# Kernel optimization log

Measured on AMD Instinct MI355X. Metric: run time of the kernel, lower is better.

## Reference

```python
import jax, jax.numpy as jnp
import numpy as np
from jax import lax

B, CIN, COUT, K, H, W = 16, 512, 512, 3, 64, 64
STYLE_DIM, BASIS, DIRS = 512, 8, 8


def setup_inputs() -> dict:
    key = jax.random.key(0)
    ks = jax.random.split(key, 8)
    return {
        "x": jax.random.normal(ks[0], (B, CIN, H, W), jnp.float32),
        "style": jax.random.normal(ks[1], (B, STYLE_DIM), jnp.float32),
        "weight": jax.random.normal(ks[2], (1, COUT, CIN, K, K), jnp.float32),
        "mod_w": jax.random.normal(ks[3], (CIN, STYLE_DIM), jnp.float32) * 0.02,
        "mod_b": jnp.ones((CIN,), jnp.float32),
        "basis_vectors": jax.random.normal(ks[4], (BASIS, 1, COUT, CIN, K, K), jnp.float32),
        "shifts_coords": jax.random.normal(ks[5], (DIRS, BASIS), jnp.float32),
        "batch_shifts": jax.random.uniform(ks[6], (B,), jnp.float32),
        "batch_directions": jax.random.randint(ks[7], (B,), 0, DIRS),
    }


def reference(x, style, weight, mod_w, mod_b, basis_vectors, shifts_coords,
              batch_shifts, batch_directions):
    batch, in_ch, h, w = x.shape
    out_ch, k = weight.shape[1], weight.shape[3]
    scale = 1.0 / np.sqrt(in_ch * k * k)  # StyleGAN2 equalized-lr scale

    # --- deformation: per-sample weight delta from basis subspace ---
    coefs = shifts_coords[batch_directions]                     # [B, basis]
    bv = basis_vectors.reshape(basis_vectors.shape[0], -1)      # [basis, O*I*k*k]
    delta = coefs @ bv                                          # [B, P]
    nrm = jnp.linalg.norm(delta, axis=1, keepdims=True)
    delta = delta / jnp.maximum(nrm, 1e-12) * batch_shifts[:, None]
    delta = delta.reshape(batch, out_ch, in_ch, k, k)
    wgt = weight + delta                                        # [B, O, I, k, k]

    # --- style modulation + demodulation ---
    s = style @ mod_w.T + mod_b                                 # [B, I]
    wgt = scale * wgt * s[:, None, :, None, None]
    demod = lax.rsqrt(jnp.sum(wgt * wgt, axis=(2, 3, 4)) + 1e-8)  # [B, O]
    wgt = wgt * demod[:, :, None, None, None]

    # --- grouped conv, groups = batch ---
    wgt = wgt.reshape(batch * out_ch, in_ch, k, k)
    xg = x.reshape(1, batch * in_ch, h, w)
    pad = k // 2
    out = lax.conv_general_dilated(
        xg, wgt, window_strides=(1, 1), padding=[(pad, pad), (pad, pad)],
        feature_group_count=batch,
        dimension_numbers=("NCHW", "OIHW", "NCHW"))
    return out.reshape(batch, out_ch, h, w)
```

## Files before the change

kernel.cpp:

```cpp
#include <hip/hip_runtime.h>


typedef __attribute__((ext_vector_type(8))) short bf16x8;
typedef __attribute__((ext_vector_type(4))) float f32x4;

__device__ __forceinline__ unsigned short f2bf(float f) {
  unsigned u = __float_as_uint(f);
  return (unsigned short)((u + 0x7FFFu + ((u >> 16) & 1u)) >> 16);
}

__device__ __forceinline__ void gl_lds16(const void* g, void* l) {
  __builtin_amdgcn_global_load_lds(
      (const __attribute__((address_space(1))) void*)g,
      (__attribute__((address_space(3))) void*)l, 16, 0, 0);
}

template <int N> __device__ __forceinline__ void vm_wait() {
  if constexpr (N == 8) asm volatile("s_waitcnt vmcnt(8)" ::: "memory");
  else if constexpr (N == 0) asm volatile("s_waitcnt vmcnt(0)" ::: "memory");
}

__global__ __launch_bounds__(256) void k_pad(const float* __restrict__ x,
                                             unsigned short* __restrict__ xp) {
  const int bx = blockIdx.x;
  const int b   = bx >> 9;
  const int rem = bx & 511;
  const int y   = rem >> 3;
  const int cb  = rem & 7;
  const int t = threadIdx.x;
  __shared__ float tile[64][65];
  const float* src = x + ((size_t)(b * 512 + cb * 64) * 4096) + y * 64;
#pragma unroll
  for (int r = 0; r < 4; ++r) {
    int idx = r * 256 + t;
    int ch = idx >> 4;
    int xq = (idx & 15) << 2;
    float4 v = *(const float4*)(src + (size_t)ch * 4096 + xq);
    tile[ch][xq + 0] = v.x; tile[ch][xq + 1] = v.y;
    tile[ch][xq + 2] = v.z; tile[ch][xq + 3] = v.w;
  }
  const uint4 z4 = {0u, 0u, 0u, 0u};
  if (t < 16) {
    const int side = t >> 3;
    const int lo = (t & 7) * 8;
    unsigned short* p =
        xp + (((size_t)(b * 66 + y + 1) * 66 + side * 65) * 512 + cb * 64 + lo);
    *(uint4*)p = z4;
  }
  if (y == 0 || y == 63) {
    const int row = (y == 0) ? 0 : 65;
    for (int idx = t; idx < 528; idx += 256) {
      const int c = idx >> 3;
      const int lo = (idx & 7) * 8;
      unsigned short* p =
          xp + (((size_t)(b * 66 + row) * 66 + c) * 512 + cb * 64 + lo);
      *(uint4*)p = z4;
    }
  }
  __syncthreads();
  const int col = t >> 2;
  const int q = t & 3;
  union { unsigned short u16[16]; uint4 v[2]; } pk;
#pragma unroll
  for (int j = 0; j < 16; ++j) pk.u16[j] = f2bf(tile[q * 16 + j][col]);
  unsigned short* dst =
      xp + (((size_t)(b * 66 + y + 1) * 66 + col + 1) * 512 + cb * 64 + q * 16);
  *(uint4*)dst = pk.v[0];
  *(uint4*)(dst + 8) = pk.v[1];
}

__global__ __launch_bounds__(256) void k_mod(const float* __restrict__ style,
                                             const float* __restrict__ mod_w,
                                             const float* __restrict__ mod_b,
                                             float* __restrict__ smod) {
  const int b = blockIdx.x;
  __shared__ float st[512];
  for (int d = threadIdx.x; d < 512; d += 256) st[d] = style[b * 512 + d];
  __syncthreads();
  for (int i = threadIdx.x; i < 512; i += 256) {
    const float* wr = mod_w + (size_t)i * 512;
    float acc = 0.f;
#pragma unroll 4
    for (int d = 0; d < 512; d += 4) {
      float4 wv = *(const float4*)(wr + d);
      acc += wv.x * st[d] + wv.y * st[d + 1] + wv.z * st[d + 2] + wv.w * st[d + 3];
    }
    smod[b * 512 + i] = acc + mod_b[i];
  }
}

__global__ __launch_bounds__(256, 3) void k_gram(const float* __restrict__ bv,
                                                 float* __restrict__ G) {
  const int P4 = 589824;
  float a[36];
#pragma unroll
  for (int c = 0; c < 36; ++c) a[c] = 0.f;
  const float4* bv4 = (const float4*)bv;
  for (int p = blockIdx.x * 256 + threadIdx.x; p < P4; p += gridDim.x * 256) {
    float4 v[8];
#pragma unroll
    for (int k = 0; k < 8; ++k) v[k] = bv4[(size_t)k * P4 + p];
    int c = 0;
#pragma unroll
    for (int i = 0; i < 8; ++i)
#pragma unroll
      for (int j = i; j < 8; ++j) {
        a[c] += v[i].x * v[j].x + v[i].y * v[j].y + v[i].z * v[j].z +
                v[i].w * v[j].w;
        ++c;
      }
  }
#pragma unroll
  for (int c = 0; c < 36; ++c)
#pragma unroll
    for (int off = 32; off > 0; off >>= 1) a[c] += __shfl_down(a[c], off);
  __shared__ float red[4][36];
  const int wv = threadIdx.x >> 6;
  if ((threadIdx.x & 63) == 0)
#pragma unroll
    for (int c = 0; c < 36; ++c) red[wv][c] = a[c];
  __syncthreads();
  if (threadIdx.x < 36)
    atomicAdd(&G[threadIdx.x], red[0][threadIdx.x] + red[1][threadIdx.x] +
                                   red[2][threadIdx.x] + red[3][threadIdx.x]);
}

__global__ void k_amp(const float* __restrict__ shifts_coords,
                      const float* __restrict__ batch_shifts,
                      const int* __restrict__ dirs, const float* __restrict__ G,
                      float* __restrict__ camp) {
  const int b = threadIdx.x;
  if (b < 16) {
    const int dir = dirs[b];
    float c[8];
    for (int k = 0; k < 8; ++k) c[k] = shifts_coords[dir * 8 + k];
    float n2 = 0.f;
    int idx = 0;
    for (int i = 0; i < 8; ++i)
      for (int j = i; j < 8; ++j) {
        float g = G[idx++];
        n2 += (i == j) ? c[i] * c[i] * g : 2.f * c[i] * c[j] * g;
      }
    float nrm = sqrtf(fmaxf(n2, 0.f));
    float amp = batch_shifts[b] / fmaxf(nrm, 1e-12f);
    for (int k = 0; k < 8; ++k) camp[b * 8 + k] = c[k] * amp;
  }
}

__global__ __launch_bounds__(512) void k_weights(const float* __restrict__ weight,
                                                 const float* __restrict__ bv,
                                                 const float* __restrict__ smod,
                                                 const float* __restrict__ camp,
                                                 unsigned short* __restrict__ wgt,
                                                 float* __restrict__ demod) {
  const int o = blockIdx.x;
  const int i = threadIdx.x;
  __shared__ float cl[128];
  __shared__ float red[8][16];
  if (threadIdx.x < 128) cl[threadIdx.x] = camp[threadIdx.x];
  __syncthreads();
  const float scl = 0.014731391274719738f;
  float sm[16];
#pragma unroll
  for (int b = 0; b < 16; ++b) sm[b] = smod[b * 512 + i] * scl;
  float ssq[16];
#pragma unroll
  for (int b = 0; b < 16; ++b) ssq[b] = 0.f;
  const size_t base = ((size_t)o * 512 + i) * 9;
#pragma unroll
  for (int g = 0; g < 3; ++g) {
    float w[3], v[8][3];
#pragma unroll
    for (int q = 0; q < 3; ++q) w[q] = weight[base + g * 3 + q];
#pragma unroll
    for (int k = 0; k < 8; ++k)
#pragma unroll
      for (int q = 0; q < 3; ++q)
        v[k][q] = bv[(size_t)k * 2359296 + base + g * 3 + q];
#pragma unroll
    for (int b = 0; b < 16; ++b) {
#pragma unroll
      for (int q = 0; q < 3; ++q) {
        float d = w[q];
#pragma unroll
        for (int k = 0; k < 8; ++k) d = fmaf(cl[b * 8 + k], v[k][q], d);
        float wv = d * sm[b];
        ssq[b] = fmaf(wv, wv, ssq[b]);
        wgt[(((size_t)(b * 9 + g * 3 + q) * 512 + o) << 9) + i] = f2bf(wv);
      }
    }
  }
#pragma unroll
  for (int b = 0; b < 16; ++b)
#pragma unroll
    for (int off = 32; off > 0; off >>= 1) ssq[b] += __shfl_down(ssq[b], off);
  const int wv_ = threadIdx.x >> 6;
  if ((threadIdx.x & 63) == 0)
#pragma unroll
    for (int b = 0; b < 16; ++b) red[wv_][b] = ssq[b];
  __syncthreads();
  if (threadIdx.x < 16) {
    float s = 0.f;
#pragma unroll
    for (int wq = 0; wq < 8; ++wq) s += red[wq][threadIdx.x];
    demod[threadIdx.x * 512 + o] = rsqrtf(s + 1e-8f);
  }
}

__global__ __launch_bounds__(512, 2) void k_conv(
    const unsigned short* __restrict__ xp, const unsigned short* __restrict__ wgt,
    const float* __restrict__ demod, float* __restrict__ out) {
  extern __shared__ unsigned char smem[];
  const int tid = threadIdx.x;
  const int l = tid & 63;
  const int w = tid >> 6;
  const int wo = w >> 2;
  const int wn = w & 3;

  const int bid = blockIdx.x;
  const int bz = (bid & 7) * 64 + (bid >> 3);
  const int b = bz >> 5;
  const int tt = bz & 31;
  const int o0 = (tt >> 4) << 8;
  const int tn = tt & 15;
  const int n0 = tn << 8;
  const int y0 = tn << 2;

  int swzS[4];
  size_t aByte[4], pBase[4];
#pragma unroll
  for (int r = 0; r < 4; ++r) {
    const int idx = r * 512 + tid;
    const int row = idx >> 3;
    const int swz = ((idx & 7) << 4) ^ ((row & 7) << 4);
    swzS[r] = swz;
    aByte[r] = ((size_t)(o0 + row) << 10) + swz;
    pBase[r] = (size_t)(b * 66 + y0 + (row >> 6)) * 66 + (row & 63);
  }

  const char* wgtc = (const char*)wgt;
  const char* xpc = (const char*)xp;

  auto stage_part = [&](unsigned char* buf, int kt, int part) {
    const int kk = kt >> 3;
    const int is = kt & 7;
    const int ky = kk / 3;
    const int kx = kk - ky * 3;
    const size_t aPlane = ((size_t)(b * 9 + kk) << 19) + ((size_t)is << 7);
    unsigned char* lA = buf;
    unsigned char* lB = buf + 32768;
    if (part == 0) {
#pragma unroll
      for (int r = 0; r < 2; ++r)
        gl_lds16(wgtc + aPlane + aByte[r], lA + (r * 512 + tid) * 16);
#pragma unroll
      for (int r = 0; r < 2; ++r)
        gl_lds16(xpc + (((pBase[r] + ky * 66 + kx) << 10) + ((size_t)is << 7) +
                        swzS[r]),
                 lB + (r * 512 + tid) * 16);
    } else if (part == 1) {
#pragma unroll
      for (int r = 2; r < 4; ++r)
        gl_lds16(xpc + (((pBase[r] + ky * 66 + kx) << 10) + ((size_t)is << 7) +
                        swzS[r]),
                 lB + (r * 512 + tid) * 16);
    } else {
#pragma unroll
      for (int r = 2; r < 4; ++r)
        gl_lds16(wgtc + aPlane + aByte[r], lA + (r * 512 + tid) * 16);
    }
  };

  f32x4 acc[8][4];
  const f32x4 zz = {0.f, 0.f, 0.f, 0.f};
#pragma unroll
  for (int mi = 0; mi < 8; ++mi)
#pragma unroll
    for (int ni = 0; ni < 4; ++ni) acc[mi][ni] = zz;
  bf16x8 af[8], bf0[4], bf1[4];

  auto rdA = [&](const unsigned char* lA, int MH) {
#pragma unroll
    for (int mi = 0; mi < 4; ++mi)
#pragma unroll
      for (int ks = 0; ks < 2; ++ks) {
        const int row = MH * 128 + wo * 64 + mi * 16 + (l & 15);
        af[mi * 2 + ks] = *(const bf16x8*)(
            lA + row * 128 + ((ks * 64 + ((l >> 4) << 4)) ^ ((row & 7) << 4)));
      }
  };
  auto rdB = [&](const unsigned char* lB, int NH, bf16x8 (&bfx)[4]) {
#pragma unroll
    for (int ni = 0; ni < 2; ++ni)
#pragma unroll
      for (int ks = 0; ks < 2; ++ks) {
        const int row = NH * 128 + wn * 32 + ni * 16 + (l & 15);
        bfx[ni * 2 + ks] = *(const bf16x8*)(
            lB + row * 128 + ((ks * 64 + ((l >> 4) << 4)) ^ ((row & 7) << 4)));
      }
  };
  auto mma = [&](int MH, int NH, bf16x8 (&bfx)[4]) {
    __builtin_amdgcn_s_setprio(1);
#pragma unroll
    for (int mi = 0; mi < 4; ++mi)
#pragma unroll
      for (int ni = 0; ni < 2; ++ni)
#pragma unroll
        for (int ks = 0; ks < 2; ++ks)
          acc[MH * 4 + mi][NH * 2 + ni] =
              __builtin_amdgcn_mfma_f32_16x16x32_bf16(
                  af[mi * 2 + ks], bfx[ni * 2 + ks],
                  acc[MH * 4 + mi][NH * 2 + ni], 0, 0, 0);
    __builtin_amdgcn_s_setprio(0);
    __builtin_amdgcn_sched_barrier(0);
  };

  stage_part(smem, 0, 0); stage_part(smem, 0, 1); stage_part(smem, 0, 2);
  stage_part(smem + 65536, 1, 0); stage_part(smem + 65536, 1, 1);
  stage_part(smem + 65536, 1, 2);
  vm_wait<8>();
  __builtin_amdgcn_s_barrier();

  int cur = 0;
#pragma unroll 1
  for (int kt = 0; kt < 72; ++kt) {
    unsigned char* lA = smem + (cur << 16);
    unsigned char* lB = lA + 32768;
    const bool stg = (kt < 70);
    rdA(lA, 0);
    rdB(lB, 0, bf0);
    __builtin_amdgcn_s_barrier();
    mma(0, 0, bf0);
    __builtin_amdgcn_s_barrier();
    __builtin_amdgcn_sched_barrier(0);
    if (stg) stage_part(lA, kt + 2, 0);
    rdB(lB, 1, bf1);
    __builtin_amdgcn_s_barrier();
    mma(0, 1, bf1);
    __builtin_amdgcn_s_barrier();
    __builtin_amdgcn_sched_barrier(0);
    if (stg) stage_part(lA, kt + 2, 1);
    rdA(lA, 1);
    __builtin_amdgcn_s_barrier();
    mma(1, 1, bf1);
    __builtin_amdgcn_s_barrier();
    __builtin_amdgcn_sched_barrier(0);
    if (stg) stage_part(lA, kt + 2, 2);
    mma(1, 0, bf0);
    if (kt < 70) vm_wait<8>();
    else if (kt == 70) vm_wait<0>();
    __builtin_amdgcn_s_barrier();
    cur ^= 1;
  }

  float* outb = out + (size_t)(b * 512 + o0) * 4096 + n0;
#pragma unroll
  for (int mh = 0; mh < 2; ++mh)
#pragma unroll
    for (int mi = 0; mi < 4; ++mi) {
      const int orow = mh * 128 + wo * 64 + mi * 16 + ((l >> 4) << 2);
      float dm[4];
#pragma unroll
      for (int r = 0; r < 4; ++r) dm[r] = demod[b * 512 + o0 + orow + r];
#pragma unroll
      for (int nh = 0; nh < 2; ++nh)
#pragma unroll
        for (int ni = 0; ni < 2; ++ni) {
          const int pix = nh * 128 + wn * 32 + ni * 16 + (l & 15);
#pragma unroll
          for (int r = 0; r < 4; ++r)
            outb[(size_t)(orow + r) * 4096 + pix] =
                acc[mh * 4 + mi][nh * 2 + ni][r] * dm[r];
        }
    }
}

extern "C" void kernel_launch(void* const* d_in, const int* in_sizes, int n_in,
                              void* d_out, int out_size, void* d_ws,
                              size_t ws_size, hipStream_t stream) {
  const float* x      = (const float*)d_in[0];
  const float* style  = (const float*)d_in[1];
  const float* weight = (const float*)d_in[2];
  const float* mod_w  = (const float*)d_in[3];
  const float* mod_b  = (const float*)d_in[4];
  const float* bv     = (const float*)d_in[5];
  const float* sc     = (const float*)d_in[6];
  const float* bsh    = (const float*)d_in[7];
  const int*   bdir   = (const int*)d_in[8];
  float* out = (float*)d_out;

  char* ws = (char*)d_ws;
  unsigned short* xp  = (unsigned short*)(ws);
  unsigned short* wgt = (unsigned short*)(ws + 71368704);
  float* G     = (float*)(ws + 146866176);
  float* camp  = (float*)(ws + 146866432);
  float* smod  = (float*)(ws + 146866944);
  float* demod = (float*)(ws + 146899712);

  hipFuncSetAttribute((const void*)k_conv,
                      hipFuncAttributeMaxDynamicSharedMemorySize, 131072);

  hipMemsetAsync(G, 0, 256, stream);
  k_pad<<<8192, 256, 0, stream>>>(x, xp);
  k_mod<<<16, 256, 0, stream>>>(style, mod_w, mod_b, smod);
  k_gram<<<1024, 256, 0, stream>>>(bv, G);
  k_amp<<<1, 64, 0, stream>>>(sc, bsh, bdir, G, camp);
  k_weights<<<512, 512, 0, stream>>>(weight, bv, smod, camp, wgt, demod);
  k_conv<<<512, 512, 131072, stream>>>(xp, wgt, demod, out);
}
```

Before: 431.9 us.

## Restructure main loop: read all fragments up front, single barrier, one-shot staging

```diff
diff --git a/kernel.cpp b/kernel.cpp
--- a/kernel.cpp
+++ b/kernel.cpp
@@ -241,7 +241,7 @@
   const char* wgtc = (const char*)wgt;
   const char* xpc = (const char*)xp;
 
-  auto stage_part = [&](unsigned char* buf, int kt, int part) {
+  auto stage_all = [&](unsigned char* buf, int kt) {
     const int kk = kt >> 3;
     const int is = kt & 7;
     const int ky = kk / 3;
@@ -249,26 +249,14 @@
     const size_t aPlane = ((size_t)(b * 9 + kk) << 19) + ((size_t)is << 7);
     unsigned char* lA = buf;
     unsigned char* lB = buf + 32768;
-    if (part == 0) {
-#pragma unroll
-      for (int r = 0; r < 2; ++r)
-        gl_lds16(wgtc + aPlane + aByte[r], lA + (r * 512 + tid) * 16);
-#pragma unroll
-      for (int r = 0; r < 2; ++r)
-        gl_lds16(xpc + (((pBase[r] + ky * 66 + kx) << 10) + ((size_t)is << 7) +
-                        swzS[r]),
-                 lB + (r * 512 + tid) * 16);
-    } else if (part == 1) {
-#pragma unroll
-      for (int r = 2; r < 4; ++r)
-        gl_lds16(xpc + (((pBase[r] + ky * 66 + kx) << 10) + ((size_t)is << 7) +
-                        swzS[r]),
-                 lB + (r * 512 + tid) * 16);
-    } else {
-#pragma unroll
-      for (int r = 2; r < 4; ++r)
-        gl_lds16(wgtc + aPlane + aByte[r], lA + (r * 512 + tid) * 16);
-    }
+#pragma unroll
+    for (int r = 0; r < 4; ++r)
+      gl_lds16(wgtc + aPlane + aByte[r], lA + (r * 512 + tid) * 16);
+#pragma unroll
+    for (int r = 0; r < 4; ++r)
+      gl_lds16(xpc + (((pBase[r] + ky * 66 + kx) << 10) + ((size_t)is << 7) +
+                      swzS[r]),
+               lB + (r * 512 + tid) * 16);
   };
 
   f32x4 acc[8][4];
@@ -277,15 +265,15 @@
   for (int mi = 0; mi < 8; ++mi)
 #pragma unroll
     for (int ni = 0; ni < 4; ++ni) acc[mi][ni] = zz;
-  bf16x8 af[8], bf0[4], bf1[4];
-
-  auto rdA = [&](const unsigned char* lA, int MH) {
+  bf16x8 af0[8], af1[8], bf0[4], bf1[4];
+
+  auto rdA = [&](const unsigned char* lA, int MH, bf16x8 (&afx)[8]) {
 #pragma unroll
     for (int mi = 0; mi < 4; ++mi)
 #pragma unroll
       for (int ks = 0; ks < 2; ++ks) {
         const int row = MH * 128 + wo * 64 + mi * 16 + (l & 15);
-        af[mi * 2 + ks] = *(const bf16x8*)(
+        afx[mi * 2 + ks] = *(const bf16x8*)(
             lA + row * 128 + ((ks * 64 + ((l >> 4) << 4)) ^ ((row & 7) << 4)));
       }
   };
@@ -299,7 +287,7 @@
             lB + row * 128 + ((ks * 64 + ((l >> 4) << 4)) ^ ((row & 7) << 4)));
       }
   };
-  auto mma = [&](int MH, int NH, bf16x8 (&bfx)[4]) {
+  auto mma = [&](int MH, int NH, bf16x8 (&afx)[8], bf16x8 (&bfx)[4]) {
     __builtin_amdgcn_s_setprio(1);
 #pragma unroll
     for (int mi = 0; mi < 4; ++mi)
@@ -309,15 +297,13 @@
         for (int ks = 0; ks < 2; ++ks)
           acc[MH * 4 + mi][NH * 2 + ni] =
               __builtin_amdgcn_mfma_f32_16x16x32_bf16(
-                  af[mi * 2 + ks], bfx[ni * 2 + ks],
+                  afx[mi * 2 + ks], bfx[ni * 2 + ks],
                   acc[MH * 4 + mi][NH * 2 + ni], 0, 0, 0);
     __builtin_amdgcn_s_setprio(0);
-    __builtin_amdgcn_sched_barrier(0);
   };
 
-  stage_part(smem, 0, 0); stage_part(smem, 0, 1); stage_part(smem, 0, 2);
-  stage_part(smem + 65536, 1, 0); stage_part(smem + 65536, 1, 1);
-  stage_part(smem + 65536, 1, 2);
+  stage_all(smem, 0);
+  stage_all(smem + 65536, 1);
   vm_wait<8>();
   __builtin_amdgcn_s_barrier();
 
@@ -326,30 +312,28 @@
   for (int kt = 0; kt < 72; ++kt) {
     unsigned char* lA = smem + (cur << 16);
     unsigned char* lB = lA + 32768;
-    const bool stg = (kt < 70);
-    rdA(lA, 0);
+    rdA(lA, 0, af0);
     rdB(lB, 0, bf0);
-    __builtin_amdgcn_s_barrier();
-    mma(0, 0, bf0);
+    rdB(lB, 1, bf1);
+    rdA(lA, 1, af1);
+    mma(0, 0, af0, bf0);
+    mma(0, 1, af0, bf1);
+    asm volatile("s_waitcnt lgkmcnt(0)" ::: "memory");
+    __builtin_amdgcn_sched_barrier(0);
     __builtin_amdgcn_s_barrier();
     __builtin_amdgcn_sched_barrier(0);
-    if (stg) stage_part(lA, kt + 2, 0);
-    rdB(lB, 1, bf1);
-    __builtin_amdgcn_s_barrier();
-    mma(0, 1, bf1);
-    __builtin_amdgcn_s_barrier();
-    __builtin_amdgcn_sched_barrier(0);
-    if (stg) stage_part(lA, kt + 2, 1);
-    rdA(lA, 1);
-    __builtin_amdgcn_s_barrier();
-    mma(1, 1, bf1);
-    __builtin_amdgcn_s_barrier();
-    __builtin_amdgcn_sched_barrier(0);
-    if (stg) stage_part(lA, kt + 2, 2);
-    mma(1, 0, bf0);
-    if (kt < 70) vm_wait<8>();
-    else if (kt == 70) vm_wait<0>();
-    __builtin_amdgcn_s_barrier();
+    if (kt < 70) stage_all(lA, kt + 2);
+    mma(1, 1, af1, bf1);
+    mma(1, 0, af1, bf0);
+    if (kt < 70) {
+      vm_wait<8>();
+      __builtin_amdgcn_s_barrier();
+      __builtin_amdgcn_sched_barrier(0);
+    } else if (kt == 70) {
+      vm_wait<0>();
+      __builtin_amdgcn_s_barrier();
+      __builtin_amdgcn_sched_barrier(0);
+    }
     cur ^= 1;
   }
 
```

New measurement: 418.2 us. -3.2%, faster.
